# Kernel tuning notes

Hardware: AMD Instinct MI355X
Metric: run time of the kernel (lower is better)

## Reference

```python
import jax, jax.numpy as jnp
import numpy as np

B, S, HID = 1, 2048, 2048
H = 16
D_NOPE, D_ROPE, D_V = 128, 64, 128
Q_HEAD = D_NOPE + D_ROPE  # 192
QL, KVL = 1536, 512
EPS = 1e-6
SCALE = Q_HEAD ** -0.5


def rms_norm(x, w, eps=EPS):
    return x * jax.lax.rsqrt(jnp.mean(x * x, axis=-1, keepdims=True) + eps) * w


def rotate_half(x):
    h = x.shape[-1] // 2
    return jnp.concatenate([-x[..., h:], x[..., :h]], axis=-1)


def apply_rope(x, cos, sin):
    # DeepSeek de-interleave: view(..., d//2, 2).transpose(-1,-2).reshape == [even, odd]
    x = jnp.concatenate([x[..., 0::2], x[..., 1::2]], axis=-1)
    return x * cos + rotate_half(x) * sin


def setup_inputs() -> dict:
    key = jax.random.key(0)
    ks = jax.random.split(key, 8)
    x = jax.random.normal(ks[0], (B, S, HID), dtype=jnp.float32)
    # causal additive mask
    causal = jnp.tril(jnp.ones((S, S), dtype=bool))
    mask = jnp.where(causal, 0.0, -1e9).astype(jnp.float32)[None, None]
    position_ids = jnp.broadcast_to(jnp.arange(S, dtype=jnp.int32), (B, S))
    # RoPE caches, theta=10000
    inv_freq = 1.0 / (10000.0 ** (np.arange(0, D_ROPE, 2, dtype=np.float32) / D_ROPE))
    freqs = np.outer(np.arange(S, dtype=np.float32), inv_freq)
    emb = np.concatenate([freqs, freqs], axis=-1)
    cos = jnp.asarray(np.cos(emb), dtype=jnp.float32)
    sin = jnp.asarray(np.sin(emb), dtype=jnp.float32)
    w = lambda k, shp: (jax.random.normal(k, shp, dtype=jnp.float32) * 0.02)
    return {
        "x": x, "mask": mask, "position_ids": position_ids, "cos": cos, "sin": sin,
        "q_a_w": w(ks[1], (HID, QL)),
        "q_a_ln": jnp.ones((QL,), jnp.float32),
        "q_b_w": w(ks[2], (QL, H * Q_HEAD)),
        "kv_a_w": w(ks[3], (HID, KVL + D_ROPE)),
        "kv_a_ln": jnp.ones((KVL,), jnp.float32),
        "kv_b_w": w(ks[4], (KVL, H * (D_NOPE + D_V))),
        "o_w": w(ks[5], (H * D_V, HID)),
    }


def reference(x, mask, position_ids, cos, sin, q_a_w, q_a_ln, q_b_w, kv_a_w, kv_a_ln, kv_b_w, o_w):
    b, s, _ = x.shape
    # low-rank Q projection
    q = rms_norm(x @ q_a_w, q_a_ln) @ q_b_w            # [B,S,H*192]
    q = q.reshape(b, s, H, Q_HEAD).transpose(0, 2, 1, 3)  # [B,H,S,192]
    q_nope, q_pe = q[..., :D_NOPE], q[..., D_NOPE:]
    # compressed KV + decoupled rope key (MQA, shared across heads)
    ckv = x @ kv_a_w                                   # [B,S,512+64]
    c_norm = rms_norm(ckv[..., :KVL], kv_a_ln)         # [B,S,512]
    k_pe = ckv[..., KVL:][:, None]                     # [B,1,S,64]
    kv = (c_norm @ kv_b_w).reshape(b, s, H, D_NOPE + D_V).transpose(0, 2, 1, 3)
    k_nope, value = kv[..., :D_NOPE], kv[..., D_NOPE:]  # [B,H,S,128] each
    # rope
    cos_p = cos[position_ids][:, None]                 # [B,1,S,64]
    sin_p = sin[position_ids][:, None]
    q_pe = apply_rope(q_pe, cos_p, sin_p)
    k_pe = apply_rope(k_pe, cos_p, sin_p)
    query = jnp.concatenate([q_nope, q_pe], axis=-1)   # [B,H,S,192]
    key = jnp.concatenate([k_nope, jnp.broadcast_to(k_pe, (b, H, s, D_ROPE))], axis=-1)
    scores = jnp.einsum("bhsd,bhtd->bhst", query, key) * SCALE + mask
    attn = jax.nn.softmax(scores, axis=-1)
    out = jnp.einsum("bhst,bhtd->bhsd", attn, value)   # [B,H,S,128]
    out = out.transpose(0, 2, 1, 3).reshape(b, s, H * D_V) @ o_w
    kv_cache = jnp.concatenate([c_norm, k_pe[:, 0]], axis=-1)  # [B,S,576] latent cache
    return out, kv_cache
```

## Files before the change

kernel.cpp:

```cpp
#include <hip/hip_runtime.h>

typedef unsigned short u16;
typedef __bf16 bf16x8 __attribute__((ext_vector_type(8)));
typedef short s16x4 __attribute__((ext_vector_type(4)));
typedef short s16x8 __attribute__((ext_vector_type(8)));
typedef float f32x4 __attribute__((ext_vector_type(4)));

#define S_LEN 2048
#define NHEAD 16
#define QHEAD 192
#define EPS 1e-6f
#define ATTN_SCALE 0.07216878364870323f
#define QSCALE_LOG2E 0.10412011228586118f

__device__ __forceinline__ u16 f2bf(float f) {
    unsigned u = __builtin_bit_cast(unsigned, f);
    u = (u + 0x7FFFu + ((u >> 16) & 1u)) >> 16;
    return (u16)u;
}
__device__ __forceinline__ float bf2f(u16 h) {
    unsigned u = ((unsigned)h) << 16;
    return __builtin_bit_cast(float, u);
}

__device__ __forceinline__ void gl_lds16(const u16* g, u16* l) {
    __builtin_amdgcn_global_load_lds(
        (const __attribute__((address_space(1))) unsigned int*)g,
        (__attribute__((address_space(3))) unsigned int*)l,
        16, 0, 0);
}

#if defined(__has_builtin) && __has_builtin(__builtin_amdgcn_mfma_f32_16x16x16bf16_1k)
__device__ __forceinline__ f32x4 mfma16(s16x4 a, s16x4 b, f32x4 c) {
    return __builtin_amdgcn_mfma_f32_16x16x16bf16_1k(a, b, c, 0, 0, 0);
}
#else
__device__ __forceinline__ f32x4 mfma16(s16x4 a, s16x4 b, f32x4 c) {
    asm volatile("v_mfma_f32_16x16x16_bf16 %0, %1, %2, %0"
                 : "+v"(c) : "v"(a), "v"(b));
    return c;
}
#endif

template <int CF32>
__device__ __forceinline__ void gemm_core(
    u16* __restrict__ smem,
    const u16* __restrict__ A, const u16* __restrict__ B, void* __restrict__ Cv,
    int K, int lda, int ldb, int ldc, int tm, int tn)
{
    const int tid = threadIdx.x;
    const int w = tid >> 6, lane = tid & 63;
    const int q = lane >> 4, r = lane & 15;

    const int lr = lane & 15;
    const int lc = (lane >> 4) * 8;
    const u16* ga0 = A + (long)(tm * 128 + w * 32 + lr) * lda + lc;
    const u16* ga1 = ga0 + 16 * (long)lda;
    const u16* gb0 = B + (long)(tn * 128 + w * 32 + lr) * ldb + lc;
    const u16* gb1 = gb0 + 16 * (long)ldb;
    const int sa0 = w * 1024, sa1 = sa0 + 512;
    const int sb0 = 4096 + w * 1024, sb1 = sb0 + 512;

    f32x4 acc[4][4] = {};
    const int wm = w >> 1;
    const int wn = w & 1;
    const int n = K >> 6;

    gl_lds16(ga0, smem + sa0);
    gl_lds16(ga1, smem + sa1);
    gl_lds16(gb0, smem + sb0);
    gl_lds16(gb1, smem + sb1);
    gl_lds16(ga0 + 32, smem + 8192 + sa0);
    gl_lds16(ga1 + 32, smem + 8192 + sa1);
    gl_lds16(gb0 + 32, smem + 8192 + sb0);
    gl_lds16(gb1 + 32, smem + 8192 + sb1);
    asm volatile("s_waitcnt vmcnt(0)" ::: "memory");
    __builtin_amdgcn_sched_barrier(0);
    __builtin_amdgcn_s_barrier();
    __builtin_amdgcn_sched_barrier(0);

    for (int t = 0; t < n; ++t) {
        u16* const cur = smem + (t & 1) * 16384;
        u16* const nxt = smem + ((t + 1) & 1) * 16384;
        if (t + 1 < n) {
            const long k1 = (long)(t + 1) << 6;
            gl_lds16(ga0 + k1, nxt + sa0);
            gl_lds16(ga1 + k1, nxt + sa1);
            gl_lds16(gb0 + k1, nxt + sb0);
            gl_lds16(gb1 + k1, nxt + sb1);
            gl_lds16(ga0 + k1 + 32, nxt + 8192 + sa0);
            gl_lds16(ga1 + k1 + 32, nxt + 8192 + sa1);
            gl_lds16(gb0 + k1 + 32, nxt + 8192 + sb0);
            gl_lds16(gb1 + k1 + 32, nxt + 8192 + sb1);
        }
        #pragma unroll
        for (int kk = 0; kk < 2; ++kk) {
            u16* const sub = cur + kk * 8192;
            bf16x8 af[4], bv[4];
            #pragma unroll
            for (int mt = 0; mt < 4; ++mt)
                af[mt] = *(const bf16x8*)&sub[(wm * 4 + mt) * 512 + lane * 8];
            #pragma unroll
            for (int nt = 0; nt < 4; ++nt)
                bv[nt] = *(const bf16x8*)&sub[4096 + (wn * 4 + nt) * 512 + lane * 8];
            #pragma unroll
            for (int mt = 0; mt < 4; ++mt)
                #pragma unroll
                for (int nt = 0; nt < 4; ++nt)
                    acc[mt][nt] = __builtin_amdgcn_mfma_f32_16x16x32_bf16(
                        af[mt], bv[nt], acc[mt][nt], 0, 0, 0);
        }
        if (t + 1 < n) {
            asm volatile("s_waitcnt vmcnt(0)" ::: "memory");
            __builtin_amdgcn_sched_barrier(0);
            __builtin_amdgcn_s_barrier();
            __builtin_amdgcn_sched_barrier(0);
        }
    }

    const int row0 = tm * 128 + wm * 64 + q * 4;
    const int col0 = tn * 128 + wn * 64 + r;
    if (CF32) {
        float* C = (float*)Cv;
        #pragma unroll
        for (int mt = 0; mt < 4; ++mt)
            #pragma unroll
            for (int i = 0; i < 4; ++i) {
                long rb = (long)(row0 + mt * 16 + i) * ldc + col0;
                #pragma unroll
                for (int nt = 0; nt < 4; ++nt)
                    C[rb + nt * 16] = acc[mt][nt][i];
            }
    } else {
        u16* C = (u16*)Cv;
        #pragma unroll
        for (int mt = 0; mt < 4; ++mt)
            #pragma unroll
            for (int i = 0; i < 4; ++i) {
                long rb = (long)(row0 + mt * 16 + i) * ldc + col0;
                #pragma unroll
                for (int nt = 0; nt < 4; ++nt)
                    C[rb + nt * 16] = f2bf(acc[mt][nt][i]);
            }
    }
}

__device__ __forceinline__ void wtrans_body(
    float (*tile)[33], const float* __restrict__ in, u16* __restrict__ out,
    int K, int N, int bx, int by, int tid)
{
    const int tx = tid & 31, ty = tid >> 5;
    const int k0 = bx * 32, n0 = by * 32;
    #pragma unroll
    for (int jj = 0; jj < 32; jj += 8) {
        int nn = n0 + tx;
        tile[ty + jj][tx] = (nn < N) ? in[(long)(k0 + ty + jj) * N + nn] : 0.0f;
    }
    __syncthreads();
    #pragma unroll
    for (int jj = 0; jj < 32; jj += 8)
        out[(long)(n0 + ty + jj) * K + k0 + tx] = f2bf(tile[tx][ty + jj]);
}

__global__ __launch_bounds__(256, 2)
void gemm_ks(const u16* __restrict__ A, const u16* __restrict__ B,
             float* __restrict__ C0, float* __restrict__ C1,
             int Kh, int lda, int ldb, int ldc)
{
    __shared__ __align__(16) u16 smem[2 * 16384];
    const int z = blockIdx.z;
    float* C = z ? C1 : C0;
    gemm_core<1>(smem, A + (long)z * Kh, B + (long)z * Kh, C,
                 Kh, lda, ldb, ldc, blockIdx.y, blockIdx.x);
}

__global__ __launch_bounds__(256, 2)
void gemm_bt_dual(const u16* __restrict__ A0, const u16* __restrict__ B0,
                  void* __restrict__ C0, int K0, int lda0, int ldb0, int ldc0, int nx0,
                  const u16* __restrict__ A1, const u16* __restrict__ B1,
                  void* __restrict__ C1, int K1, int lda1, int ldb1, int ldc1, int nx1)
{
    __shared__ __align__(16) u16 smem[2 * 16384];
    if (blockIdx.z == 0) {
        if ((int)blockIdx.x >= nx0) return;
        gemm_core<0>(smem, A0, B0, C0, K0, lda0, ldb0, ldc0,
                     blockIdx.y, blockIdx.x);
    } else {
        if ((int)blockIdx.x >= nx1) return;
        gemm_core<0>(smem, A1, B1, C1, K1, lda1, ldb1, ldc1,
                     blockIdx.y, blockIdx.x);
    }
}

__global__ __launch_bounds__(256)
void addout_k(float4* __restrict__ out, const float4* __restrict__ p)
{
    int i = blockIdx.x * 256 + threadIdx.x;
    float4 a = out[i], b = p[i];
    a.x += b.x; a.y += b.y; a.z += b.z; a.w += b.w;
    out[i] = a;
}

template<int C0, int C1>
__device__ __forceinline__ void stage_tile(
    const u16* __restrict__ kvb, const u16* __restrict__ kpe,
    const u16* __restrict__ vt,
    u16* __restrict__ Kl, u16* __restrict__ Vl,
    int h, int t, int quad, int r)
{
    #pragma unroll
    for (int c = C0; c < C1; ++c) {
        if (c < 24) {
            const int mtk = c / 6, kc = c % 6;
            const int row = t * 64 + mtk * 16 + r;
            const u16* src = (kc < 4)
                ? kvb + (size_t)row * 4096 + h * 256 + kc * 32 + quad * 8
                : kpe + (size_t)row * 64 + (kc - 4) * 32 + quad * 8;
            gl_lds16(src, &Kl[c * 512]);
        } else {
            const int cv = c - 24, mtd = cv >> 1, sc = cv & 1;
            const u16* src = vt + ((size_t)h * 128 + mtd * 16 + r) * 2048
                             + t * 64 + sc * 32 + quad * 8;
            gl_lds16(src, &Vl[cv * 512]);
        }
    }
}

__device__ __forceinline__ void stage_dispatch(
    const u16* __restrict__ kvb, const u16* __restrict__ kpe,
    const u16* __restrict__ vt,
    u16* __restrict__ Kl, u16* __restrict__ Vl,
    int w, int h, int t, int quad, int r)
{
    if (w == 0)      stage_tile<0, 10>(kvb, kpe, vt, Kl, Vl, h, t, quad, r);
    else if (w == 1) stage_tile<10, 20>(kvb, kpe, vt, Kl, Vl, h, t, quad, r);
    else if (w == 2) stage_tile<20, 30>(kvb, kpe, vt, Kl, Vl, h, t, quad, r);
    else             stage_tile<30, 40>(kvb, kpe, vt, Kl, Vl, h, t, quad, r);
}

__device__ __forceinline__ void kv_tile_step(
    const u16* __restrict__ Kl, const u16* __restrict__ Vl,
    const bf16x8 (&Qf)[6], f32x4 (&Oacc)[8], float& lsum,
    int lane, int quad, int r, int kglob0, int qg, bool maskT)
{
    __builtin_amdgcn_s_setprio(1);
    f32x4 Sacc[4];
    #pragma unroll
    for (int mtk = 0; mtk < 4; ++mtk)
        Sacc[mtk] = (f32x4){0.f, 0.f, 0.f, 0.f};
    #pragma unroll
    for (int kc = 0; kc < 6; ++kc)
        #pragma unroll
        for (int mtk = 0; mtk < 4; ++mtk) {
            bf16x8 Ak = *(const bf16x8*)&Kl[(mtk * 6 + kc) * 512 + lane * 8];
            Sacc[mtk] = __builtin_amdgcn_mfma_f32_16x16x32_bf16(
                Ak, Qf[kc], Sacc[mtk], 0, 0, 0);
        }
    #pragma unroll
    for (int sc = 0; sc < 2; ++sc) {
        s16x4 Pf[2];
        #pragma unroll
        for (int half = 0; half < 2; ++half) {
            const int kb = sc * 2 + half;
            const int kb0 = kglob0 + kb * 16 + quad * 4;
            #pragma unroll
            for (int i = 0; i < 4; ++i) {
                float pv = exp2f(Sacc[kb][i]);
                if (maskT && (kb0 + i > qg)) pv = 0.f;
                lsum += pv;
                Pf[half][i] = (short)f2bf(pv);
            }
        }
        #pragma unroll
        for (int mtd = 0; mtd < 8; ++mtd) {
            s16x8 Av8 = *(const s16x8*)&Vl[(mtd * 2 + sc) * 512 + quad * 128 + r * 8];
            s16x4 lo = __builtin_shufflevector(Av8, Av8, 0, 1, 2, 3);
            s16x4 hi = __builtin_shufflevector(Av8, Av8, 4, 5, 6, 7);
            Oacc[mtd] = mfma16(lo, Pf[0], Oacc[mtd]);
            Oacc[mtd] = mfma16(hi, Pf[1], Oacc[mtd]);
        }
    }
    __builtin_amdgcn_s_setprio(0);
}

__global__ __launch_bounds__(256, 2)
void flash_attn(const u16* __restrict__ query, const u16* __restrict__ kvb,
                const u16* __restrict__ kpe, const u16* __restrict__ vt,
                float* __restrict__ PA, float* __restrict__ PB,
                float* __restrict__ lp)
{
    const int tid = threadIdx.x;
    const int w = tid >> 6, lane = tid & 63;
    const int quad = lane >> 4, r = lane & 15;

    const int bid = (int)blockIdx.x;
    const int hf = bid >> 9;
    const int p = bid & 511;
    const int i = p & 255;
    const int t_ = i >> 4;
    const int h = i & 15;
    const int j = (p < 256) ? (31 - t_) : t_;

    const int q0 = j * 64;
    const int nfull = j + 1;
    const int sp = (nfull + 1) >> 1;
    const int t0 = hf ? sp : 0;
    const int t1 = hf ? nfull : sp;

    __shared__ __align__(16) u16 smem[40960];

    const int qg = q0 + w * 16 + r;

    bf16x8 Qf[6];
    #pragma unroll
    for (int kc = 0; kc < 6; ++kc)
        Qf[kc] = *(const bf16x8*)(query
            + ((size_t)h * S_LEN + q0 + w * 16 + r) * QHEAD
            + kc * 32 + quad * 8);

    f32x4 Oacc[8];
    #pragma unroll
    for (int mtd = 0; mtd < 8; ++mtd)
        Oacc[mtd] = (f32x4){0.f, 0.f, 0.f, 0.f};
    float lsum = 0.f;

    if (t0 < t1)
        stage_dispatch(kvb, kpe, vt, smem, smem + 12288, w, h, t0, quad, r);
    __syncthreads();

    for (int t = t0; t < t1; ++t) {
        u16* const curb = smem + ((t - t0) & 1) * 20480;
        u16* const nxtb = smem + ((t - t0 + 1) & 1) * 20480;
        if (t + 1 < t1)
            stage_dispatch(kvb, kpe, vt, nxtb, nxtb + 12288, w, h, t + 1, quad, r);
        kv_tile_step(curb, curb + 12288, Qf, Oacc, lsum,
                     lane, quad, r, t * 64, qg, t == nfull - 1);
        __syncthreads();
    }

    float l = lsum;
    l += __shfl_xor(l, 16, 64);
    l += __shfl_xor(l, 32, 64);
    float* OP = hf ? PB : PA;
    const long pb = ((long)p * 64 + w * 16 + r) * 128;
    #pragma unroll
    for (int mtd = 0; mtd < 8; ++mtd)
        *(f32x4*)&OP[pb + mtd * 16 + quad * 4] = Oacc[mtd];
    if (quad == 0)
        lp[hf * 32768 + p * 64 + w * 16 + r] = l;
}

__global__ __launch_bounds__(256)
void merge_k(const float* __restrict__ PA, const float* __restrict__ PB,
             const float* __restrict__ lp, u16* __restrict__ ao)
{
    const int p = (int)blockIdx.x, tid = threadIdx.x;
    const int i = p & 255;
    const int t_ = i >> 4;
    const int h = i & 15;
    const int j = (p < 256) ? (31 - t_) : t_;
    const int q0 = j * 64;
    const int row = tid >> 2;
    const int cseg = (tid & 3) * 32;
    const float lA = lp[p * 64 + row];
    const float lB = lp[32768 + p * 64 + row];
    const float inv = 1.0f / (lA + lB);
    const long base = ((long)p * 64 + row) * 128 + cseg;
    u16* dst = ao + (size_t)(q0 + row) * 2048 + h * 128 + cseg;
    #pragma unroll
    for (int k = 0; k < 8; ++k) {
        f32x4 va = *(const f32x4*)&PA[base + k * 4];
        f32x4 vb = *(const f32x4*)&PB[base + k * 4];
        ushort4 o;
        o.x = f2bf((va[0] + vb[0]) * inv);
        o.y = f2bf((va[1] + vb[1]) * inv);
        o.z = f2bf((va[2] + vb[2]) * inv);
        o.w = f2bf((va[3] + vb[3]) * inv);
        *(ushort4*)(dst + k * 4) = o;
    }
}

__global__ __launch_bounds__(256)
void prep_k(const float4* __restrict__ x4, ushort4* __restrict__ xb4,
            const float* __restrict__ q_a_w, const float* __restrict__ kv_a_w,
            const float* __restrict__ q_b_w, const float* __restrict__ kv_b_w,
            const float* __restrict__ o_w,
            u16* __restrict__ W1, u16* __restrict__ qbwt,
            u16* __restrict__ kvbwt, u16* __restrict__ owt)
{
    __shared__ float tile[32][33];
    const int tid = threadIdx.x;
    int b = (int)blockIdx.x;
    if (b < 4096) {
        int i = b * 256 + tid;
        float4 v = x4[i];
        ushort4 o;
        o.x = f2bf(v.x); o.y = f2bf(v.y); o.z = f2bf(v.z); o.w = f2bf(v.w);
        xb4[i] = o;
        return;
    }
    b -= 4096;
    if (b < 3072)       wtrans_body(tile, q_a_w,  W1,                  2048, 1536, b % 64, b / 64, tid);
    else if ((b -= 3072) < 1280) wtrans_body(tile, kv_a_w, W1 + 1536ULL * 2048, 2048, 576,  b % 64, b / 64, tid);
    else if ((b -= 1280) < 4608) wtrans_body(tile, q_b_w,  qbwt,       1536, 3072, b % 48, b / 48, tid);
    else if ((b -= 4608) < 2048) wtrans_body(tile, kv_b_w, kvbwt,      512,  4096, b % 16, b / 16, tid);
    else { b -= 2048;            wtrans_body(tile, o_w,    owt,        2048, 2048, b % 64, b / 64, tid); }
}

__global__ __launch_bounds__(256)
void norm_k(const float* __restrict__ pa, const float* __restrict__ pb,
            u16* __restrict__ qkv, const float* __restrict__ q_ln,
            const float* __restrict__ kv_ln, const int* __restrict__ pos_ids,
            const float* __restrict__ cosb, const float* __restrict__ sinb,
            float* __restrict__ kvout, u16* __restrict__ cnb,
            u16* __restrict__ kpe)
{
    const int s = blockIdx.x, tid = threadIdx.x;
    __shared__ float rowbuf[2176];
    __shared__ float red[8];
    const long base = (long)s * 2176;
    float sum1 = 0.f, sum2 = 0.f;
    for (int d = tid; d < 2176; d += 256) {
        float v = pa[base + d] + pb[base + d];
        rowbuf[d] = v;
        if (d < 1536)      sum1 += v * v;
        else if (d < 2048) sum2 += v * v;
    }
    #pragma unroll
    for (int o = 32; o; o >>= 1) {
        sum1 += __shfl_xor(sum1, o, 64);
        sum2 += __shfl_xor(sum2, o, 64);
    }
    if ((tid & 63) == 0) { red[tid >> 6] = sum1; red[4 + (tid >> 6)] = sum2; }
    __syncthreads();
    sum1 = red[0] + red[1] + red[2] + red[3];
    sum2 = red[4] + red[5] + red[6] + red[7];
    const float sc1 = rsqrtf(sum1 / 1536.f + EPS);
    const float sc2 = rsqrtf(sum2 / 512.f + EPS);
    for (int d = tid; d < 1536; d += 256)
        qkv[base + d] = f2bf(rowbuf[d] * sc1 * q_ln[d]);
    for (int d = tid; d < 512; d += 256) {
        float v = rowbuf[1536 + d] * sc2 * kv_ln[d];
        kvout[(long)s * 576 + d] = v;
        cnb[(long)s * 512 + d] = f2bf(v);
    }
    if (tid < 32) {
        int p = pos_ids[s];
        float x0 = rowbuf[2048 + 2 * tid];
        float x1 = rowbuf[2048 + 2 * tid + 1];
        float c1 = cosb[p * 64 + tid], s1 = sinb[p * 64 + tid];
        float c2 = cosb[p * 64 + 32 + tid], s2 = sinb[p * 64 + 32 + tid];
        float lo = x0 * c1 - x1 * s1;
        float hi = x1 * c2 + x0 * s2;
        kvout[(long)s * 576 + 512 + tid] = lo;
        kvout[(long)s * 576 + 544 + tid] = hi;
        kpe[(long)s * 64 + tid] = f2bf(lo);
        kpe[(long)s * 64 + 32 + tid] = f2bf(hi);
    }
}

__global__ __launch_bounds__(256)
void post_k(const u16* __restrict__ qb, const int* __restrict__ pos_ids,
            const float* __restrict__ cosb, const float* __restrict__ sinb,
            u16* __restrict__ query, const u16* __restrict__ kv,
            u16* __restrict__ vt)
{
    __shared__ u16 tile[32][33];
    const int tid = threadIdx.x;
    int b = (int)blockIdx.x;
    if (b < 2048) {
        const int s = b;
        const u16* row = qb + (long)s * 3072;
        {
            int h = tid >> 4, c = tid & 15;
            const u16* src = &row[h * QHEAD + c * 8];
            u16* dst = &query[((long)(h * S_LEN + s)) * QHEAD + c * 8];
            ushort4 a = *(const ushort4*)src;
            ushort4 bb = *(const ushort4*)(src + 4);
            ushort4 oa, ob;
            oa.x = f2bf(bf2f(a.x) * QSCALE_LOG2E); oa.y = f2bf(bf2f(a.y) * QSCALE_LOG2E);
            oa.z = f2bf(bf2f(a.z) * QSCALE_LOG2E); oa.w = f2bf(bf2f(a.w) * QSCALE_LOG2E);
            ob.x = f2bf(bf2f(bb.x) * QSCALE_LOG2E); ob.y = f2bf(bf2f(bb.y) * QSCALE_LOG2E);
            ob.z = f2bf(bf2f(bb.z) * QSCALE_LOG2E); ob.w = f2bf(bf2f(bb.w) * QSCALE_LOG2E);
            *(ushort4*)dst = oa;
            *(ushort4*)(dst + 4) = ob;
        }
        int p = pos_ids[s];
        for (int idx = tid; idx < 512; idx += 256) {
            int h = idx >> 5, i = idx & 31;
            float x0 = bf2f(row[h * QHEAD + 128 + 2 * i]);
            float x1 = bf2f(row[h * QHEAD + 128 + 2 * i + 1]);
            float c1 = cosb[p * 64 + i], s1 = sinb[p * 64 + i];
            float c2 = cosb[p * 64 + 32 + i], s2 = sinb[p * 64 + 32 + i];
            u16* qr = query + ((long)(h * S_LEN + s)) * QHEAD;
            qr[128 + i] = f2bf((x0 * c1 - x1 * s1) * QSCALE_LOG2E);
            qr[160 + i] = f2bf((x1 * c2 + x0 * s2) * QSCALE_LOG2E);
        }
    } else {
        b -= 2048;
        const int s0 = (b & 63) * 32, d0 = ((b >> 6) & 3) * 32, h = b >> 8;
        const int tx = tid & 31, ty = tid >> 5;
        #pragma unroll
        for (int jj = 0; jj < 32; jj += 8)
            tile[ty + jj][tx] = kv[(long)(s0 + ty + jj) * 4096 + h * 256 + 128 + d0 + tx];
        __syncthreads();
        const int txp = ((tx >> 2) & 3) * 8 + (tx >> 4) * 4 + (tx & 3);
        #pragma unroll
        for (int jj = 0; jj < 32; jj += 8)
            vt[(long)(h * 128 + d0 + ty + jj) * S_LEN + s0 + txp] = tile[tx][ty + jj];
    }
}

extern "C" void kernel_launch(void* const* d_in, const int* in_sizes, int n_in,
                              void* d_out, int out_size, void* d_ws, size_t ws_size,
                              hipStream_t stream)
{
    const float* x      = (const float*)d_in[0];
    const int*   posid  = (const int*)d_in[2];
    const float* cosb   = (const float*)d_in[3];
    const float* sinb   = (const float*)d_in[4];
    const float* q_a_w  = (const float*)d_in[5];
    const float* q_a_ln = (const float*)d_in[6];
    const float* q_b_w  = (const float*)d_in[7];
    const float* kv_a_w = (const float*)d_in[8];
    const float* kv_a_ln= (const float*)d_in[9];
    const float* kv_b_w = (const float*)d_in[10];
    const float* o_w    = (const float*)d_in[11];

    float* out    = (float*)d_out;
    float* kv_out = out + (size_t)2048 * 2048;

    char* ws = (char*)d_ws;
    size_t off = 0;
    auto alloc = [&](size_t bytes) { char* p = ws + off; off += (bytes + 255) & ~(size_t)255; return p; };
    u16* xb    = (u16*)alloc(2048ULL * 2048 * 2);
    u16* W1    = (u16*)alloc(2176ULL * 2048 * 2);
    u16* owt   = (u16*)alloc(2048ULL * 2048 * 2);
    u16* qbwt  = (u16*)alloc(3072ULL * 1536 * 2);
    u16* kvbwt = (u16*)alloc(4096ULL * 512 * 2);
    u16* qkv_a = (u16*)alloc(2048ULL * 2176 * 2);
    u16* qbuf  = (u16*)alloc(2048ULL * 3072 * 2);
    u16* query = (u16*)alloc(16ULL * 2048 * 192 * 2);
    u16* cnb   = (u16*)alloc(2048ULL * 512 * 2);
    u16* kpe   = (u16*)alloc(2048ULL * 64 * 2);
    u16* kvbuf = (u16*)alloc(2048ULL * 4096 * 2);
    u16* vt    = (u16*)alloc(16ULL * 128 * 2048 * 2);
    u16* ao    = (u16*)alloc(2048ULL * 2048 * 2);
    (void)ws_size; (void)in_sizes; (void)n_in; (void)out_size;

    float* g1p0 = (float*)qbuf;
    float* g1p1 = (float*)kvbuf;
    float* PA   = (float*)xb;
    float* PB   = (float*)qbwt;
    float* lp   = (float*)cnb;
    float* g5p  = (float*)xb;

    dim3 blk(256);

    prep_k<<<dim3(19200), blk, 0, stream>>>(
        (const float4*)x, (ushort4*)xb, q_a_w, kv_a_w, q_b_w, kv_b_w, o_w,
        W1, qbwt, kvbwt, owt);

    gemm_ks<<<dim3(17, 16, 2), blk, 0, stream>>>(
        xb, W1, g1p0, g1p1, 1024, 2048, 2048, 2176);

    norm_k<<<dim3(2048), blk, 0, stream>>>(g1p0, g1p1, qkv_a, q_a_ln, kv_a_ln,
                                           posid, cosb, sinb, kv_out, cnb, kpe);

    gemm_bt_dual<<<dim3(32, 16, 2), blk, 0, stream>>>(
        qkv_a, qbwt, qbuf, 1536, 2176, 1536, 3072, 24,
        cnb, kvbwt, kvbuf, 512, 512, 512, 4096, 32);

    post_k<<<dim3(6144), blk, 0, stream>>>(qbuf, posid, cosb, sinb, query, kvbuf, vt);

    flash_attn<<<dim3(1024), blk, 0, stream>>>(query, kvbuf, kpe, vt, PA, PB, lp);

    merge_k<<<dim3(512), blk, 0, stream>>>(PA, PB, lp, ao);

    gemm_ks<<<dim3(16, 16, 2), blk, 0, stream>>>(
        ao, owt, g5p, out, 1024, 2048, 2048, 2048);
    addout_k<<<dim3(4096), blk, 0, stream>>>((float4*)out, (const float4*)g5p);
}
```

Before: 398.6 us.

## Triple-buffer GEMM with K=32 stages and halve attention KV tile to raise occupancy

```diff
diff --git a/kernel.cpp b/kernel.cpp
--- a/kernel.cpp
+++ b/kernel.cpp
@@ -64,7 +64,7 @@
     f32x4 acc[4][4] = {};
     const int wm = w >> 1;
     const int wn = w & 1;
-    const int n = K >> 6;
+    const int n = K >> 5;
 
     gl_lds16(ga0, smem + sa0);
     gl_lds16(ga1, smem + sa1);
@@ -74,48 +74,44 @@
     gl_lds16(ga1 + 32, smem + 8192 + sa1);
     gl_lds16(gb0 + 32, smem + 8192 + sb0);
     gl_lds16(gb1 + 32, smem + 8192 + sb1);
-    asm volatile("s_waitcnt vmcnt(0)" ::: "memory");
+    asm volatile("s_waitcnt vmcnt(4)" ::: "memory");
     __builtin_amdgcn_sched_barrier(0);
     __builtin_amdgcn_s_barrier();
     __builtin_amdgcn_sched_barrier(0);
 
+    int bc = 0;
     for (int t = 0; t < n; ++t) {
-        u16* const cur = smem + (t & 1) * 16384;
-        u16* const nxt = smem + ((t + 1) & 1) * 16384;
-        if (t + 1 < n) {
-            const long k1 = (long)(t + 1) << 6;
-            gl_lds16(ga0 + k1, nxt + sa0);
-            gl_lds16(ga1 + k1, nxt + sa1);
-            gl_lds16(gb0 + k1, nxt + sb0);
-            gl_lds16(gb1 + k1, nxt + sb1);
-            gl_lds16(ga0 + k1 + 32, nxt + 8192 + sa0);
-            gl_lds16(ga1 + k1 + 32, nxt + 8192 + sa1);
-            gl_lds16(gb0 + k1 + 32, nxt + 8192 + sb0);
-            gl_lds16(gb1 + k1 + 32, nxt + 8192 + sb1);
-        }
-        #pragma unroll
-        for (int kk = 0; kk < 2; ++kk) {
-            u16* const sub = cur + kk * 8192;
-            bf16x8 af[4], bv[4];
-            #pragma unroll
-            for (int mt = 0; mt < 4; ++mt)
-                af[mt] = *(const bf16x8*)&sub[(wm * 4 + mt) * 512 + lane * 8];
+        u16* const cur = smem + bc * 8192;
+        if (t + 2 < n) {
+            int bn = bc + 2; if (bn >= 3) bn -= 3;
+            u16* const nxt = smem + bn * 8192;
+            const long k2 = (long)(t + 2) << 5;
+            gl_lds16(ga0 + k2, nxt + sa0);
+            gl_lds16(ga1 + k2, nxt + sa1);
+            gl_lds16(gb0 + k2, nxt + sb0);
+            gl_lds16(gb1 + k2, nxt + sb1);
+        }
+        bf16x8 af[4], bv[4];
+        #pragma unroll
+        for (int mt = 0; mt < 4; ++mt)
+            af[mt] = *(const bf16x8*)&cur[(wm * 4 + mt) * 512 + lane * 8];
+        #pragma unroll
+        for (int nt = 0; nt < 4; ++nt)
+            bv[nt] = *(const bf16x8*)&cur[4096 + (wn * 4 + nt) * 512 + lane * 8];
+        #pragma unroll
+        for (int mt = 0; mt < 4; ++mt)
             #pragma unroll
             for (int nt = 0; nt < 4; ++nt)
-                bv[nt] = *(const bf16x8*)&sub[4096 + (wn * 4 + nt) * 512 + lane * 8];
-            #pragma unroll
-            for (int mt = 0; mt < 4; ++mt)
-                #pragma unroll
-                for (int nt = 0; nt < 4; ++nt)
-                    acc[mt][nt] = __builtin_amdgcn_mfma_f32_16x16x32_bf16(
-                        af[mt], bv[nt], acc[mt][nt], 0, 0, 0);
-        }
+                acc[mt][nt] = __builtin_amdgcn_mfma_f32_16x16x32_bf16(
+                    af[mt], bv[nt], acc[mt][nt], 0, 0, 0);
         if (t + 1 < n) {
-            asm volatile("s_waitcnt vmcnt(0)" ::: "memory");
+            if (t + 2 < n) asm volatile("s_waitcnt vmcnt(4)" ::: "memory");
+            else           asm volatile("s_waitcnt vmcnt(0)" ::: "memory");
             __builtin_amdgcn_sched_barrier(0);
             __builtin_amdgcn_s_barrier();
             __builtin_amdgcn_sched_barrier(0);
         }
+        if (++bc == 3) bc = 0;
     }
 
     const int row0 = tm * 128 + wm * 64 + q * 4;
@@ -167,7 +163,7 @@
              float* __restrict__ C0, float* __restrict__ C1,
              int Kh, int lda, int ldb, int ldc)
 {
-    __shared__ __align__(16) u16 smem[2 * 16384];
+    __shared__ __align__(16) u16 smem[3 * 8192];
     const int z = blockIdx.z;
     float* C = z ? C1 : C0;
     gemm_core<1>(smem, A + (long)z * Kh, B + (long)z * Kh, C,
@@ -180,7 +176,7 @@
                   const u16* __restrict__ A1, const u16* __restrict__ B1,
                   void* __restrict__ C1, int K1, int lda1, int ldb1, int ldc1, int nx1)
 {
-    __shared__ __align__(16) u16 smem[2 * 16384];
+    __shared__ __align__(16) u16 smem[3 * 8192];
     if (blockIdx.z == 0) {
         if ((int)blockIdx.x >= nx0) return;
         gemm_core<0>(smem, A0, B0, C0, K0, lda0, ldb0, ldc0,
@@ -202,7 +198,7 @@
 }
 
 template<int C0, int C1>
-__device__ __forceinline__ void stage_tile(
+__device__ __forceinline__ void stage_tile32(
     const u16* __restrict__ kvb, const u16* __restrict__ kpe,
     const u16* __restrict__ vt,
     u16* __restrict__ Kl, u16* __restrict__ Vl,
@@ -210,80 +206,75 @@
 {
     #pragma unroll
     for (int c = C0; c < C1; ++c) {
-        if (c < 24) {
+        if (c < 12) {
             const int mtk = c / 6, kc = c % 6;
-            const int row = t * 64 + mtk * 16 + r;
+            const int row = t * 32 + mtk * 16 + r;
             const u16* src = (kc < 4)
                 ? kvb + (size_t)row * 4096 + h * 256 + kc * 32 + quad * 8
                 : kpe + (size_t)row * 64 + (kc - 4) * 32 + quad * 8;
             gl_lds16(src, &Kl[c * 512]);
         } else {
-            const int cv = c - 24, mtd = cv >> 1, sc = cv & 1;
+            const int mtd = c - 12;
             const u16* src = vt + ((size_t)h * 128 + mtd * 16 + r) * 2048
-                             + t * 64 + sc * 32 + quad * 8;
-            gl_lds16(src, &Vl[cv * 512]);
-        }
-    }
-}
-
-__device__ __forceinline__ void stage_dispatch(
+                             + t * 32 + quad * 8;
+            gl_lds16(src, &Vl[mtd * 512]);
+        }
+    }
+}
+
+__device__ __forceinline__ void stage_dispatch32(
     const u16* __restrict__ kvb, const u16* __restrict__ kpe,
     const u16* __restrict__ vt,
     u16* __restrict__ Kl, u16* __restrict__ Vl,
     int w, int h, int t, int quad, int r)
 {
-    if (w == 0)      stage_tile<0, 10>(kvb, kpe, vt, Kl, Vl, h, t, quad, r);
-    else if (w == 1) stage_tile<10, 20>(kvb, kpe, vt, Kl, Vl, h, t, quad, r);
-    else if (w == 2) stage_tile<20, 30>(kvb, kpe, vt, Kl, Vl, h, t, quad, r);
-    else             stage_tile<30, 40>(kvb, kpe, vt, Kl, Vl, h, t, quad, r);
-}
-
-__device__ __forceinline__ void kv_tile_step(
+    if (w == 0)      stage_tile32<0, 5>(kvb, kpe, vt, Kl, Vl, h, t, quad, r);
+    else if (w == 1) stage_tile32<5, 10>(kvb, kpe, vt, Kl, Vl, h, t, quad, r);
+    else if (w == 2) stage_tile32<10, 15>(kvb, kpe, vt, Kl, Vl, h, t, quad, r);
+    else             stage_tile32<15, 20>(kvb, kpe, vt, Kl, Vl, h, t, quad, r);
+}
+
+__device__ __forceinline__ void kv_tile_step32(
     const u16* __restrict__ Kl, const u16* __restrict__ Vl,
     const bf16x8 (&Qf)[6], f32x4 (&Oacc)[8], float& lsum,
     int lane, int quad, int r, int kglob0, int qg, bool maskT)
 {
     __builtin_amdgcn_s_setprio(1);
-    f32x4 Sacc[4];
-    #pragma unroll
-    for (int mtk = 0; mtk < 4; ++mtk)
-        Sacc[mtk] = (f32x4){0.f, 0.f, 0.f, 0.f};
+    f32x4 Sacc[2];
+    Sacc[0] = (f32x4){0.f, 0.f, 0.f, 0.f};
+    Sacc[1] = (f32x4){0.f, 0.f, 0.f, 0.f};
     #pragma unroll
     for (int kc = 0; kc < 6; ++kc)
         #pragma unroll
-        for (int mtk = 0; mtk < 4; ++mtk) {
+        for (int mtk = 0; mtk < 2; ++mtk) {
             bf16x8 Ak = *(const bf16x8*)&Kl[(mtk * 6 + kc) * 512 + lane * 8];
             Sacc[mtk] = __builtin_amdgcn_mfma_f32_16x16x32_bf16(
                 Ak, Qf[kc], Sacc[mtk], 0, 0, 0);
         }
-    #pragma unroll
-    for (int sc = 0; sc < 2; ++sc) {
-        s16x4 Pf[2];
-        #pragma unroll
-        for (int half = 0; half < 2; ++half) {
-            const int kb = sc * 2 + half;
-            const int kb0 = kglob0 + kb * 16 + quad * 4;
-            #pragma unroll
-            for (int i = 0; i < 4; ++i) {
-                float pv = exp2f(Sacc[kb][i]);
-                if (maskT && (kb0 + i > qg)) pv = 0.f;
-                lsum += pv;
-                Pf[half][i] = (short)f2bf(pv);
-            }
-        }
-        #pragma unroll
-        for (int mtd = 0; mtd < 8; ++mtd) {
-            s16x8 Av8 = *(const s16x8*)&Vl[(mtd * 2 + sc) * 512 + quad * 128 + r * 8];
-            s16x4 lo = __builtin_shufflevector(Av8, Av8, 0, 1, 2, 3);
-            s16x4 hi = __builtin_shufflevector(Av8, Av8, 4, 5, 6, 7);
-            Oacc[mtd] = mfma16(lo, Pf[0], Oacc[mtd]);
-            Oacc[mtd] = mfma16(hi, Pf[1], Oacc[mtd]);
-        }
+    s16x4 Pf[2];
+    #pragma unroll
+    for (int kb = 0; kb < 2; ++kb) {
+        const int kb0 = kglob0 + kb * 16 + quad * 4;
+        #pragma unroll
+        for (int i = 0; i < 4; ++i) {
+            float pv = exp2f(Sacc[kb][i]);
+            if (maskT && (kb0 + i > qg)) pv = 0.f;
+            lsum += pv;
+            Pf[kb][i] = (short)f2bf(pv);
+        }
+    }
+    #pragma unroll
+    for (int mtd = 0; mtd < 8; ++mtd) {
+        s16x8 Av8 = *(const s16x8*)&Vl[mtd * 512 + quad * 128 + r * 8];
+        s16x4 lo = __builtin_shufflevector(Av8, Av8, 0, 1, 2, 3);
+        s16x4 hi = __builtin_shufflevector(Av8, Av8, 4, 5, 6, 7);
+        Oacc[mtd] = mfma16(lo, Pf[0], Oacc[mtd]);
+        Oacc[mtd] = mfma16(hi, Pf[1], Oacc[mtd]);
     }
     __builtin_amdgcn_s_setprio(0);
 }
 
-__global__ __launch_bounds__(256, 2)
+__global__ __launch_bounds__(256, 4)
 void flash_attn(const u16* __restrict__ query, const u16* __restrict__ kvb,
                 const u16* __restrict__ kpe, const u16* __restrict__ vt,
                 float* __restrict__ PA, float* __restrict__ PB,
@@ -302,12 +293,12 @@
     const int j = (p < 256) ? (31 - t_) : t_;
 
     const int q0 = j * 64;
-    const int nfull = j + 1;
-    const int sp = (nfull + 1) >> 1;
+    const int ntk = 2 * (j + 1);
+    const int sp = j + 1;
     const int t0 = hf ? sp : 0;
-    const int t1 = hf ? nfull : sp;
-
-    __shared__ __align__(16) u16 smem[40960];
+    const int t1 = hf ? ntk : sp;
+
+    __shared__ __align__(16) u16 smem[20480];
 
     const int qg = q0 + w * 16 + r;
 
@@ -324,17 +315,16 @@
         Oacc[mtd] = (f32x4){0.f, 0.f, 0.f, 0.f};
     float lsum = 0.f;
 
-    if (t0 < t1)
-        stage_dispatch(kvb, kpe, vt, smem, smem + 12288, w, h, t0, quad, r);
+    stage_dispatch32(kvb, kpe, vt, smem, smem + 6144, w, h, t0, quad, r);
     __syncthreads();
 
     for (int t = t0; t < t1; ++t) {
-        u16* const curb = smem + ((t - t0) & 1) * 20480;
-        u16* const nxtb = smem + ((t - t0 + 1) & 1) * 20480;
+        u16* const curb = smem + ((t - t0) & 1) * 10240;
+        u16* const nxtb = smem + ((t - t0 + 1) & 1) * 10240;
         if (t + 1 < t1)
-            stage_dispatch(kvb, kpe, vt, nxtb, nxtb + 12288, w, h, t + 1, quad, r);
-        kv_tile_step(curb, curb + 12288, Qf, Oacc, lsum,
-                     lane, quad, r, t * 64, qg, t == nfull - 1);
+            stage_dispatch32(kvb, kpe, vt, nxtb, nxtb + 6144, w, h, t + 1, quad, r);
+        kv_tile_step32(curb, curb + 6144, Qf, Oacc, lsum,
+                       lane, quad, r, t * 32, qg, t >= ntk - 2);
         __syncthreads();
     }
 
```

After: 380.2 us. 4.6% less time.
